# Kernel optimization log

Hardware: AMD Instinct MI355X
Metric: run time of the kernel (lower is better)

## Reference

```python
import jax, jax.numpy as jnp
import numpy as np

N_NODES = 100000
N_EDGES = 1600000


def setup_inputs() -> dict:
    key = jax.random.key(0)
    k1, k2, k3, k4 = jax.random.split(key, 4)
    x = jax.random.normal(k1, (N_NODES, 256), dtype=jnp.float32)
    edge_index = jax.random.randint(k2, (2, N_EDGES), 0, N_NODES, dtype=jnp.int64)
    W1 = jax.random.normal(k3, (256, 128), dtype=jnp.float32) * (1.0 / np.sqrt(256))
    W2 = jax.random.normal(k4, (128, 40), dtype=jnp.float32) * (1.0 / np.sqrt(128))
    return {"x": x, "edge_index": edge_index, "W1": W1, "W2": W2}


def _gcn_conv(x, W, src, dst):
    # GCNConv(normalize=False, add_self_loops=False, bias=False):
    # linear transform then sum-aggregate messages along edges src->dst.
    h = x @ W                                   # [N, d_out]
    msg = h[src]                                # [E, d_out] gather
    return jax.ops.segment_sum(msg, dst, num_segments=N_NODES)  # [N, d_out] scatter-add


def reference(x, edge_index, W1, W2):
    src, dst = edge_index[0], edge_index[1]
    h = jax.nn.relu(_gcn_conv(x, W1, src, dst))
    # dropout is identity in eval mode
    out = _gcn_conv(h, W2, src, dst)
    return out
```

## Files before the change

### kernel.cpp

```cpp
#include <hip/hip_runtime.h>

constexpr int NN = 100000;
constexpr int NE = 1600000;
constexpr int DI = 256, DH = 128, DO = 40;

constexpr int NB = (NN + 255) >> 8;
constexpr int NB_BLK = 512;
constexpr int CHUNK = NE / NB_BLK;
constexpr int M2 = NB * NB_BLK;
constexpr int NBS = (M2 + 1023) / 1024;
constexpr int STAGE_CAP = 6144;
constexpr int WPACK_BLOCKS = 152;
constexpr int GEMM1_BLOCKS = (NN + 63) / 64;

typedef __attribute__((ext_vector_type(8))) __bf16 bf16x8;
typedef __attribute__((ext_vector_type(4))) float f32x4;

__device__ inline float4 bf4_to_f4(ushort4 u) {
    return make_float4(__builtin_bit_cast(float, (unsigned)u.x << 16),
                       __builtin_bit_cast(float, (unsigned)u.y << 16),
                       __builtin_bit_cast(float, (unsigned)u.z << 16),
                       __builtin_bit_cast(float, (unsigned)u.w << 16));
}
__device__ inline unsigned short f2bf(float f) {
    return __builtin_bit_cast(unsigned short, (__bf16)f);
}
__device__ inline bf16x8 bf16x8_zero() {
    bf16x8 r;
    #pragma unroll
    for (int j = 0; j < 8; ++j) r[j] = (__bf16)0.f;
    return r;
}
__device__ inline bf16x8 load_cvt_a(const float* __restrict__ p, bool ok) {
    if (!ok) return bf16x8_zero();
    bf16x8 r;
    const float4 v0 = *(const float4*)p;
    const float4 v1 = *(const float4*)(p + 4);
    r[0] = (__bf16)v0.x; r[1] = (__bf16)v0.y; r[2] = (__bf16)v0.z; r[3] = (__bf16)v0.w;
    r[4] = (__bf16)v1.x; r[5] = (__bf16)v1.y; r[6] = (__bf16)v1.z; r[7] = (__bf16)v1.w;
    return r;
}
__device__ inline void acc4(float4& a, float4 v) {
    a.x += v.x; a.y += v.y; a.z += v.z; a.w += v.w;
}

__global__ __launch_bounds__(256) void wpack_hist_kernel(const float* __restrict__ W1,
                                                         const float* __restrict__ W2,
                                                         const int* __restrict__ dst,
                                                         __bf16* __restrict__ Wf,
                                                         __bf16* __restrict__ Wf2,
                                                         int* __restrict__ hist2d) {
    __shared__ int h[NB];
    if (blockIdx.x < 128) {
        const int i = blockIdx.x * 256 + threadIdx.x;
        const int j = i & 7;
        const int lane = (i >> 3) & 63;
        const int nt = (i >> 9) & 7;
        const int kt = i >> 12;
        const int k = kt * 32 + (lane >> 4) * 8 + j;
        const int n = nt * 16 + (lane & 15);
        Wf[i] = (__bf16)W1[(size_t)k * DH + n];
    } else if (blockIdx.x < WPACK_BLOCKS) {
        const int i = (blockIdx.x - 128) * 256 + threadIdx.x;
        if (i < 6144) {
            const int j = i & 7;
            const int lane = (i >> 3) & 63;
            const int g = i >> 9;
            const int nt = g % 3, ks = g / 3;
            const int k = ks * 32 + (lane >> 4) * 8 + j;
            const int n = nt * 16 + (lane & 15);
            Wf2[i] = (n < DO) ? (__bf16)W2[(size_t)k * DO + n] : (__bf16)0.f;
        }
    } else {
        const int hb = blockIdx.x - WPACK_BLOCKS;
        for (int i = threadIdx.x; i < NB; i += 256) h[i] = 0;
        __syncthreads();
        const int base = hb * CHUNK;
        for (int i = threadIdx.x; i < CHUNK; i += 256)
            atomicAdd(&h[dst[base + i] >> 8], 1);
        __syncthreads();
        for (int i = threadIdx.x; i < NB; i += 256)
            hist2d[i * NB_BLK + hb] = h[i];
    }
}

__global__ __launch_bounds__(256) void gemm1_scan_kernel(const float* __restrict__ x,
                                                         const __bf16* __restrict__ Wf,
                                                         __bf16* __restrict__ h1,
                                                         const int* __restrict__ hist2d,
                                                         int* __restrict__ offs2d) {
    __shared__ __bf16 wlds[32768];
    if (blockIdx.x >= NBS) {
        const int t = threadIdx.x;
        const int wave = t >> 6, lane = t & 63;
        const int q = lane >> 4, m = lane & 15;
        const int row0 = (blockIdx.x - NBS) * 64 + wave * 16;
        const int r = row0 + m;
        const bool ok = r < NN;
        const float* xp = x + (size_t)r * DI;

        bf16x8 a[8];
        #pragma unroll
        for (int kt = 0; kt < 8; ++kt)
            a[kt] = load_cvt_a(xp + kt * 32 + q * 8, ok);

        bf16x8* wl = (bf16x8*)wlds;
        const bf16x8* wfv = (const bf16x8*)Wf;
        #pragma unroll
        for (int i = 0; i < 16; ++i)
            wl[t + i * 256] = wfv[t + i * 256];

        f32x4 acc[8];
        #pragma unroll
        for (int nt = 0; nt < 8; ++nt)
            #pragma unroll
            for (int rr = 0; rr < 4; ++rr) acc[nt][rr] = 0.f;

        __syncthreads();

        #pragma unroll
        for (int kt = 0; kt < 8; ++kt) {
            #pragma unroll
            for (int nt = 0; nt < 8; ++nt) {
                const bf16x8 b = wl[(kt * 8 + nt) * 64 + lane];
                acc[nt] = __builtin_amdgcn_mfma_f32_16x16x32_bf16(a[kt], b, acc[nt], 0, 0, 0);
            }
        }
        #pragma unroll
        for (int reg = 0; reg < 4; ++reg) {
            const int rr = row0 + q * 4 + reg;
            if (rr < NN) {
                __bf16* hp = h1 + (size_t)rr * DH + m;
                #pragma unroll
                for (int nt = 0; nt < 8; ++nt) hp[nt * 16] = (__bf16)acc[nt][reg];
            }
        }
    } else {
        int* red = (int*)wlds;
        const int b = blockIdx.x;
        const int t = threadIdx.x;
        int s = 0;
        const int limit = b * 1024;
        for (int i = t * 4; i < limit; i += 1024) {
            const int4 v = *(const int4*)(hist2d + i);
            s += v.x + v.y + v.z + v.w;
        }
        red[t] = s;
        __syncthreads();
        #pragma unroll
        for (int d = 128; d > 0; d >>= 1) {
            if (t < d) red[t] += red[t + d];
            __syncthreads();
        }
        const int base = red[0];
        __syncthreads();
        const int idx = b * 1024 + t * 4;
        int4 v = make_int4(0, 0, 0, 0);
        if (idx < M2) v = *(const int4*)(hist2d + idx);
        const int sl = v.x + v.y + v.z + v.w;
        red[t] = sl;
        __syncthreads();
        for (int d = 1; d < 256; d <<= 1) {
            const int u = (t >= d) ? red[t - d] : 0;
            __syncthreads();
            red[t] += u;
            __syncthreads();
        }
        if (idx < M2) {
            const int e0 = base + red[t] - sl;
            *(int4*)(offs2d + idx) = make_int4(e0, e0 + v.x, e0 + v.x + v.y,
                                               e0 + v.x + v.y + v.z);
        }
    }
}

__global__ __launch_bounds__(256) void bucket_scatter_kernel(const int* __restrict__ src,
                                                             const int* __restrict__ dst,
                                                             const int* __restrict__ offs2d,
                                                             unsigned* __restrict__ epack) {
    __shared__ int cur[NB];
    for (int i = threadIdx.x; i < NB; i += 256)
        cur[i] = offs2d[i * NB_BLK + blockIdx.x];
    __syncthreads();
    const int base = blockIdx.x * CHUNK;
    for (int i = threadIdx.x; i < CHUNK; i += 256) {
        const int d = dst[base + i], s = src[base + i];
        const int p = atomicAdd(&cur[d >> 8], 1);
        epack[p] = (unsigned)s | ((unsigned)(d & 255) << 24);
    }
}

__global__ __launch_bounds__(256) void bucket_sort_kernel(const unsigned* __restrict__ epack,
                                                          const int* __restrict__ offs2d,
                                                          int* __restrict__ off,
                                                          int* __restrict__ esrc) {
    __shared__ int cnt[256];
    __shared__ int incl[256];
    __shared__ int cur[256];
    __shared__ int stage[STAGE_CAP];
    const int b = blockIdx.x;
    const int t = threadIdx.x;
    const int bstart = offs2d[b * NB_BLK];
    const int bend = (b + 1 < NB) ? offs2d[(b + 1) * NB_BLK] : NE;
    const int n = bend - bstart;
    cnt[t] = 0;
    __syncthreads();
    for (int i = t; i < n; i += 256)
        atomicAdd(&cnt[epack[bstart + i] >> 24], 1);
    __syncthreads();
    incl[t] = cnt[t];
    __syncthreads();
    for (int d = 1; d < 256; d <<= 1) {
        const int u = (t >= d) ? incl[t - d] : 0;
        __syncthreads();
        incl[t] += u;
        __syncthreads();
    }
    const int ex = incl[t] - cnt[t];
    const int node = (b << 8) + t;
    if (node <= NN) off[node] = bstart + ex;
    cur[t] = ex;
    __syncthreads();
    const bool staged = (n <= STAGE_CAP);
    for (int i = t; i < n; i += 256) {
        const unsigned pk = epack[bstart + i];
        const int p = atomicAdd(&cur[pk >> 24], 1);
        const int s = (int)(pk & 0xFFFFFFu);
        if (staged) stage[p] = s;
        else esrc[bstart + p] = s;
    }
    __syncthreads();
    if (staged)
        for (int i = t; i < n; i += 256) esrc[bstart + i] = stage[i];
}

__global__ __launch_bounds__(256) void agg1_kernel(const __bf16* __restrict__ h1,
                                                   const int* __restrict__ esrc,
                                                   const int* __restrict__ off,
                                                   __bf16* __restrict__ agg) {
    const int w = (blockIdx.x * 256 + threadIdx.x) >> 6;
    if (w >= NN) return;
    const int lane = threadIdx.x & 63;
    const int half = lane >> 5;
    const int c = (lane & 31) * 4;
    const int b = off[w], e = off[w + 1];
    float4 a0 = make_float4(0.f, 0.f, 0.f, 0.f);
    float4 a1 = a0, a2 = a0, a3 = a0;
    int j = b + half;
    for (; j + 6 < e; j += 8) {
        const int s0 = esrc[j], s1 = esrc[j + 2], s2 = esrc[j + 4], s3 = esrc[j + 6];
        acc4(a0, bf4_to_f4(*(const ushort4*)(h1 + (size_t)s0 * DH + c)));
        acc4(a1, bf4_to_f4(*(const ushort4*)(h1 + (size_t)s1 * DH + c)));
        acc4(a2, bf4_to_f4(*(const ushort4*)(h1 + (size_t)s2 * DH + c)));
        acc4(a3, bf4_to_f4(*(const ushort4*)(h1 + (size_t)s3 * DH + c)));
    }
    for (; j < e; j += 2) {
        const int s = esrc[j];
        acc4(a0, bf4_to_f4(*(const ushort4*)(h1 + (size_t)s * DH + c)));
    }
    float4 acc = make_float4(a0.x + a1.x + a2.x + a3.x,
                             a0.y + a1.y + a2.y + a3.y,
                             a0.z + a1.z + a2.z + a3.z,
                             a0.w + a1.w + a2.w + a3.w);
    acc.x += __shfl_xor(acc.x, 32);
    acc.y += __shfl_xor(acc.y, 32);
    acc.z += __shfl_xor(acc.z, 32);
    acc.w += __shfl_xor(acc.w, 32);
    if (half == 0) {
        ushort4 o;
        o.x = f2bf(fmaxf(acc.x, 0.f));
        o.y = f2bf(fmaxf(acc.y, 0.f));
        o.z = f2bf(fmaxf(acc.z, 0.f));
        o.w = f2bf(fmaxf(acc.w, 0.f));
        *(ushort4*)(agg + (size_t)w * DH + c) = o;
    }
}

__global__ __launch_bounds__(256) void gemm2_kernel(const __bf16* __restrict__ agg,
                                                    const __bf16* __restrict__ Wf2,
                                                    __bf16* __restrict__ h2) {
    const int t = threadIdx.x;
    const int wave = t >> 6, lane = t & 63;
    const int q = lane >> 4, m = lane & 15;
    const int row0 = blockIdx.x * 64 + wave * 16;
    const int r = row0 + m;
    const bool ok = r < NN;
    const __bf16* ap = agg + (size_t)r * DH;

    f32x4 acc[3];
    #pragma unroll
    for (int nt = 0; nt < 3; ++nt)
        #pragma unroll
        for (int rr = 0; rr < 4; ++rr) acc[nt][rr] = 0.f;

    const bf16x8* wf2 = (const bf16x8*)Wf2;
    #pragma unroll
    for (int ks = 0; ks < 4; ++ks) {
        const int k0 = ks * 32 + q * 8;
        const bf16x8 a = ok ? *(const bf16x8*)(ap + k0) : bf16x8_zero();
        #pragma unroll
        for (int nt = 0; nt < 3; ++nt) {
            const bf16x8 b = wf2[(ks * 3 + nt) * 64 + lane];
            acc[nt] = __builtin_amdgcn_mfma_f32_16x16x32_bf16(a, b, acc[nt], 0, 0, 0);
        }
    }
    #pragma unroll
    for (int reg = 0; reg < 4; ++reg) {
        const int rr = row0 + q * 4 + reg;
        if (rr < NN) {
            #pragma unroll
            for (int nt = 0; nt < 3; ++nt) {
                const int cc = nt * 16 + m;
                if (cc < DO) h2[(size_t)rr * DO + cc] = (__bf16)acc[nt][reg];
            }
        }
    }
}

__global__ __launch_bounds__(256) void agg2_kernel(const __bf16* __restrict__ h2,
                                                   const int* __restrict__ esrc,
                                                   const int* __restrict__ off,
                                                   float* __restrict__ out) {
    const int w = (blockIdx.x * 256 + threadIdx.x) >> 6;
    if (w >= NN) return;
    const int lane = threadIdx.x & 63;
    const int sub = lane / 10;
    const int c = (lane % 10) * 4;
    const int b = off[w], e = off[w + 1];
    const int deg = e - b;
    float4 a0 = make_float4(0.f, 0.f, 0.f, 0.f);
    float4 a1 = a0, a2 = a0, a3 = a0;

    for (int base = 0; base < deg; base += 64) {
        const int cnt = min(64, deg - base);
        const int cl = cnt - 1;
        const int idx = (base + lane < deg) ? esrc[b + base + lane] : 0;
        const bool act = sub < 6;
        int kk = 0;
        for (; kk + 24 <= cnt; kk += 24) {
            const int e0 = kk + sub;
            const int s0 = __shfl(idx, min(e0, cl));
            const int s1 = __shfl(idx, min(e0 + 6, cl));
            const int s2 = __shfl(idx, min(e0 + 12, cl));
            const int s3 = __shfl(idx, min(e0 + 18, cl));
            const float4 v0 = bf4_to_f4(*(const ushort4*)(h2 + (size_t)s0 * DO + c));
            const float4 v1 = bf4_to_f4(*(const ushort4*)(h2 + (size_t)s1 * DO + c));
            const float4 v2 = bf4_to_f4(*(const ushort4*)(h2 + (size_t)s2 * DO + c));
            const float4 v3 = bf4_to_f4(*(const ushort4*)(h2 + (size_t)s3 * DO + c));
            if (act) { acc4(a0, v0); acc4(a1, v1); acc4(a2, v2); acc4(a3, v3); }
        }
        for (; kk + 12 <= cnt; kk += 12) {
            const int e0 = kk + sub;
            const int s0 = __shfl(idx, min(e0, cl));
            const int s1 = __shfl(idx, min(e0 + 6, cl));
            const float4 v0 = bf4_to_f4(*(const ushort4*)(h2 + (size_t)s0 * DO + c));
            const float4 v1 = bf4_to_f4(*(const ushort4*)(h2 + (size_t)s1 * DO + c));
            if (act) { acc4(a0, v0); acc4(a1, v1); }
        }
        for (; kk < cnt; kk += 6) {
            const int e0 = kk + sub;
            const int s0 = __shfl(idx, min(e0, cl));
            const float4 v = bf4_to_f4(*(const ushort4*)(h2 + (size_t)s0 * DO + c));
            if (act && e0 < cnt) acc4(a0, v);
        }
    }
    float4 acc = make_float4(a0.x + a1.x + a2.x + a3.x, a0.y + a1.y + a2.y + a3.y,
                             a0.z + a1.z + a2.z + a3.z, a0.w + a1.w + a2.w + a3.w);
    acc.x += __shfl(acc.x, lane + 30);
    acc.y += __shfl(acc.y, lane + 30);
    acc.z += __shfl(acc.z, lane + 30);
    acc.w += __shfl(acc.w, lane + 30);
    const float ax = acc.x + __shfl(acc.x, lane + 10) + __shfl(acc.x, lane + 20);
    const float ay = acc.y + __shfl(acc.y, lane + 10) + __shfl(acc.y, lane + 20);
    const float az = acc.z + __shfl(acc.z, lane + 10) + __shfl(acc.z, lane + 20);
    const float aw = acc.w + __shfl(acc.w, lane + 10) + __shfl(acc.w, lane + 20);
    if (lane < 10) {
        *(float4*)(out + (size_t)w * DO + c) = make_float4(ax, ay, az, aw);
    }
}

extern "C" void kernel_launch(void* const* d_in, const int* in_sizes, int n_in,
                              void* d_out, int out_size, void* d_ws, size_t ws_size,
                              hipStream_t stream) {
    const float* x  = (const float*)d_in[0];
    const int*   ei = (const int*)d_in[1];
    const float* W1 = (const float*)d_in[2];
    const float* W2 = (const float*)d_in[3];
    const int* src = ei;
    const int* dst = ei + NE;

    __bf16* Wf  = (__bf16*)d_ws;
    __bf16* Wf2 = Wf + 32768;
    __bf16* h1  = Wf2 + 6144;
    __bf16* agg = h1 + (size_t)NN * DH;
    __bf16* h2  = h1;
    unsigned* epack = (unsigned*)(agg + (size_t)NN * DH);
    int* esrc   = (int*)(epack + NE);
    int* off    = esrc + NE;
    int* hist2d = off + NN + 1;
    int* offs2d = hist2d + M2;

    float* out = (float*)d_out;

    wpack_hist_kernel<<<WPACK_BLOCKS + NB_BLK, 256, 0, stream>>>(W1, W2, dst, Wf, Wf2, hist2d);
    gemm1_scan_kernel<<<GEMM1_BLOCKS + NBS, 256, 0, stream>>>(x, Wf, h1, hist2d, offs2d);
    bucket_scatter_kernel<<<NB_BLK, 256, 0, stream>>>(src, dst, offs2d, epack);
    bucket_sort_kernel<<<NB, 256, 0, stream>>>(epack, offs2d, off, esrc);
    agg1_kernel<<<(NN * 64 + 255) / 256, 256, 0, stream>>>(h1, esrc, off, agg);
    gemm2_kernel<<<(NN + 63) / 64, 256, 0, stream>>>(agg, Wf2, h2);
    agg2_kernel<<<(NN * 64 + 255) / 256, 256, 0, stream>>>(h2, esrc, off, out);
}
```

Before: 335.7 us.

## Spread GEMM1 blocks across scan, scatter and sort launches to overlap work

GEMM1 row blocks are split into three groups, and each group is folded into one of the scan, bucket-scatter and bucket-sort launches through a templated mid_kernel. The aim is to fill idle CUs during the small, latency-bound CSR-building phases with independent GEMM work, instead of running GEMM1 only alongside the scan. The cost is that every block now reserves 64KB of shared memory, which can lower occupancy for the scatter and sort blocks. The group sizes G0 and G1 are hand-tuned splits.

```diff
diff --git a/kernel.cpp b/kernel.cpp
--- a/kernel.cpp
+++ b/kernel.cpp
@@ -12,6 +12,10 @@
 constexpr int STAGE_CAP = 6144;
 constexpr int WPACK_BLOCKS = 152;
 constexpr int GEMM1_BLOCKS = (NN + 63) / 64;
+
+constexpr int G0 = 170;
+constexpr int G1 = 600;
+constexpr int G2 = GEMM1_BLOCKS - G0 - G1;
 
 typedef __attribute__((ext_vector_type(8))) __bf16 bf16x8;
 typedef __attribute__((ext_vector_type(4))) float f32x4;
@@ -84,105 +88,103 @@
     }
 }
 
-__global__ __launch_bounds__(256) void gemm1_scan_kernel(const float* __restrict__ x,
-                                                         const __bf16* __restrict__ Wf,
-                                                         __bf16* __restrict__ h1,
-                                                         const int* __restrict__ hist2d,
-                                                         int* __restrict__ offs2d) {
-    __shared__ __bf16 wlds[32768];
-    if (blockIdx.x >= NBS) {
-        const int t = threadIdx.x;
-        const int wave = t >> 6, lane = t & 63;
-        const int q = lane >> 4, m = lane & 15;
-        const int row0 = (blockIdx.x - NBS) * 64 + wave * 16;
-        const int r = row0 + m;
-        const bool ok = r < NN;
-        const float* xp = x + (size_t)r * DI;
-
-        bf16x8 a[8];
+
+__device__ inline void gemm1_body(f32x4* smem4, const float* __restrict__ x,
+                                  const __bf16* __restrict__ Wf,
+                                  __bf16* __restrict__ h1, int gb) {
+    const int t = threadIdx.x;
+    const int wave = t >> 6, lane = t & 63;
+    const int q = lane >> 4, m = lane & 15;
+    const int row0 = gb * 64 + wave * 16;
+    const int r = row0 + m;
+    const bool ok = r < NN;
+    const float* xp = x + (size_t)r * DI;
+
+    bf16x8 a[8];
+    #pragma unroll
+    for (int kt = 0; kt < 8; ++kt)
+        a[kt] = load_cvt_a(xp + kt * 32 + q * 8, ok);
+
+    bf16x8* wl = (bf16x8*)smem4;
+    const bf16x8* wfv = (const bf16x8*)Wf;
+    #pragma unroll
+    for (int i = 0; i < 16; ++i)
+        wl[t + i * 256] = wfv[t + i * 256];
+
+    f32x4 acc[8];
+    #pragma unroll
+    for (int nt = 0; nt < 8; ++nt)
         #pragma unroll
-        for (int kt = 0; kt < 8; ++kt)
-            a[kt] = load_cvt_a(xp + kt * 32 + q * 8, ok);
-
-        bf16x8* wl = (bf16x8*)wlds;
-        const bf16x8* wfv = (const bf16x8*)Wf;
+        for (int rr = 0; rr < 4; ++rr) acc[nt][rr] = 0.f;
+
+    __syncthreads();
+
+    #pragma unroll
+    for (int kt = 0; kt < 8; ++kt) {
         #pragma unroll
-        for (int i = 0; i < 16; ++i)
-            wl[t + i * 256] = wfv[t + i * 256];
-
-        f32x4 acc[8];
-        #pragma unroll
-        for (int nt = 0; nt < 8; ++nt)
+        for (int nt = 0; nt < 8; ++nt) {
+            const bf16x8 b = wl[(kt * 8 + nt) * 64 + lane];
+            acc[nt] = __builtin_amdgcn_mfma_f32_16x16x32_bf16(a[kt], b, acc[nt], 0, 0, 0);
+        }
+    }
+    #pragma unroll
+    for (int reg = 0; reg < 4; ++reg) {
+        const int rr = row0 + q * 4 + reg;
+        if (rr < NN) {
+            __bf16* hp = h1 + (size_t)rr * DH + m;
             #pragma unroll
-            for (int rr = 0; rr < 4; ++rr) acc[nt][rr] = 0.f;
-
-        __syncthreads();
-
-        #pragma unroll
-        for (int kt = 0; kt < 8; ++kt) {
-            #pragma unroll
-            for (int nt = 0; nt < 8; ++nt) {
-                const bf16x8 b = wl[(kt * 8 + nt) * 64 + lane];
-                acc[nt] = __builtin_amdgcn_mfma_f32_16x16x32_bf16(a[kt], b, acc[nt], 0, 0, 0);
-            }
-        }
-        #pragma unroll
-        for (int reg = 0; reg < 4; ++reg) {
-            const int rr = row0 + q * 4 + reg;
-            if (rr < NN) {
-                __bf16* hp = h1 + (size_t)rr * DH + m;
-                #pragma unroll
-                for (int nt = 0; nt < 8; ++nt) hp[nt * 16] = (__bf16)acc[nt][reg];
-            }
-        }
-    } else {
-        int* red = (int*)wlds;
-        const int b = blockIdx.x;
-        const int t = threadIdx.x;
-        int s = 0;
-        const int limit = b * 1024;
-        for (int i = t * 4; i < limit; i += 1024) {
-            const int4 v = *(const int4*)(hist2d + i);
-            s += v.x + v.y + v.z + v.w;
-        }
-        red[t] = s;
-        __syncthreads();
-        #pragma unroll
-        for (int d = 128; d > 0; d >>= 1) {
-            if (t < d) red[t] += red[t + d];
-            __syncthreads();
-        }
-        const int base = red[0];
-        __syncthreads();
-        const int idx = b * 1024 + t * 4;
-        int4 v = make_int4(0, 0, 0, 0);
-        if (idx < M2) v = *(const int4*)(hist2d + idx);
-        const int sl = v.x + v.y + v.z + v.w;
-        red[t] = sl;
-        __syncthreads();
-        for (int d = 1; d < 256; d <<= 1) {
-            const int u = (t >= d) ? red[t - d] : 0;
-            __syncthreads();
-            red[t] += u;
-            __syncthreads();
-        }
-        if (idx < M2) {
-            const int e0 = base + red[t] - sl;
-            *(int4*)(offs2d + idx) = make_int4(e0, e0 + v.x, e0 + v.x + v.y,
-                                               e0 + v.x + v.y + v.z);
-        }
-    }
-}
-
-__global__ __launch_bounds__(256) void bucket_scatter_kernel(const int* __restrict__ src,
-                                                             const int* __restrict__ dst,
-                                                             const int* __restrict__ offs2d,
-                                                             unsigned* __restrict__ epack) {
-    __shared__ int cur[NB];
+            for (int nt = 0; nt < 8; ++nt) hp[nt * 16] = (__bf16)acc[nt][reg];
+        }
+    }
+}
+
+__device__ inline void scan_body(f32x4* smem4, const int* __restrict__ hist2d,
+                                 int* __restrict__ offs2d, int b) {
+    int* red = (int*)smem4;
+    const int t = threadIdx.x;
+    int s = 0;
+    const int limit = b * 1024;
+    for (int i = t * 4; i < limit; i += 1024) {
+        const int4 v = *(const int4*)(hist2d + i);
+        s += v.x + v.y + v.z + v.w;
+    }
+    red[t] = s;
+    __syncthreads();
+    #pragma unroll
+    for (int d = 128; d > 0; d >>= 1) {
+        if (t < d) red[t] += red[t + d];
+        __syncthreads();
+    }
+    const int base = red[0];
+    __syncthreads();
+    const int idx = b * 1024 + t * 4;
+    int4 v = make_int4(0, 0, 0, 0);
+    if (idx < M2) v = *(const int4*)(hist2d + idx);
+    const int sl = v.x + v.y + v.z + v.w;
+    red[t] = sl;
+    __syncthreads();
+    for (int d = 1; d < 256; d <<= 1) {
+        const int u = (t >= d) ? red[t - d] : 0;
+        __syncthreads();
+        red[t] += u;
+        __syncthreads();
+    }
+    if (idx < M2) {
+        const int e0 = base + red[t] - sl;
+        *(int4*)(offs2d + idx) = make_int4(e0, e0 + v.x, e0 + v.x + v.y,
+                                           e0 + v.x + v.y + v.z);
+    }
+}
+
+__device__ inline void scatter_body(f32x4* smem4, const int* __restrict__ src,
+                                    const int* __restrict__ dst,
+                                    const int* __restrict__ offs2d,
+                                    unsigned* __restrict__ epack, int hb) {
+    int* cur = (int*)smem4;
     for (int i = threadIdx.x; i < NB; i += 256)
-        cur[i] = offs2d[i * NB_BLK + blockIdx.x];
-    __syncthreads();
-    const int base = blockIdx.x * CHUNK;
+        cur[i] = offs2d[i * NB_BLK + hb];
+    __syncthreads();
+    const int base = hb * CHUNK;
     for (int i = threadIdx.x; i < CHUNK; i += 256) {
         const int d = dst[base + i], s = src[base + i];
         const int p = atomicAdd(&cur[d >> 8], 1);
@@ -190,15 +192,13 @@
     }
 }
 
-__global__ __launch_bounds__(256) void bucket_sort_kernel(const unsigned* __restrict__ epack,
-                                                          const int* __restrict__ offs2d,
-                                                          int* __restrict__ off,
-                                                          int* __restrict__ esrc) {
-    __shared__ int cnt[256];
-    __shared__ int incl[256];
-    __shared__ int cur[256];
-    __shared__ int stage[STAGE_CAP];
-    const int b = blockIdx.x;
+__device__ inline void sort_body(f32x4* smem4, const unsigned* __restrict__ epack,
+                                 const int* __restrict__ offs2d,
+                                 int* __restrict__ off, int* __restrict__ esrc, int b) {
+    int* cnt  = (int*)smem4;
+    int* incl = cnt + 256;
+    int* cur  = incl + 256;
+    int* stage = cur + 256;
     const int t = threadIdx.x;
     const int bstart = offs2d[b * NB_BLK];
     const int bend = (b + 1 < NB) ? offs2d[(b + 1) * NB_BLK] : NE;
@@ -232,6 +232,28 @@
     __syncthreads();
     if (staged)
         for (int i = t; i < n; i += 256) esrc[bstart + i] = stage[i];
+}
+
+template<int PHASE, int CHAIN, int GBASE>
+__global__ __launch_bounds__(256) void mid_kernel(const float* __restrict__ x,
+                                                  const __bf16* __restrict__ Wf,
+                                                  __bf16* __restrict__ h1,
+                                                  const int* __restrict__ hist2d,
+                                                  int* __restrict__ offs2d,
+                                                  const int* __restrict__ src,
+                                                  const int* __restrict__ dst,
+                                                  unsigned* __restrict__ epack,
+                                                  int* __restrict__ off,
+                                                  int* __restrict__ esrc) {
+    __shared__ f32x4 smem4[4096];
+    const int b = blockIdx.x;
+    if (b < CHAIN) {
+        if constexpr (PHASE == 0) scan_body(smem4, hist2d, offs2d, b);
+        else if constexpr (PHASE == 1) scatter_body(smem4, src, dst, offs2d, epack, b);
+        else sort_body(smem4, epack, offs2d, off, esrc, b);
+    } else {
+        gemm1_body(smem4, x, Wf, h1, GBASE + (b - CHAIN));
+    }
 }
 
 __global__ __launch_bounds__(256) void agg1_kernel(const __bf16* __restrict__ h1,
@@ -403,9 +425,12 @@
     float* out = (float*)d_out;
 
     wpack_hist_kernel<<<WPACK_BLOCKS + NB_BLK, 256, 0, stream>>>(W1, W2, dst, Wf, Wf2, hist2d);
-    gemm1_scan_kernel<<<GEMM1_BLOCKS + NBS, 256, 0, stream>>>(x, Wf, h1, hist2d, offs2d);
-    bucket_scatter_kernel<<<NB_BLK, 256, 0, stream>>>(src, dst, offs2d, epack);
-    bucket_sort_kernel<<<NB, 256, 0, stream>>>(epack, offs2d, off, esrc);
+    mid_kernel<0, NBS, 0><<<NBS + G0, 256, 0, stream>>>(
+        x, Wf, h1, hist2d, offs2d, src, dst, epack, off, esrc);
+    mid_kernel<1, NB_BLK, G0><<<NB_BLK + G1, 256, 0, stream>>>(
+        x, Wf, h1, hist2d, offs2d, src, dst, epack, off, esrc);
+    mid_kernel<2, NB, G0 + G1><<<NB + G2, 256, 0, stream>>>(
+        x, Wf, h1, hist2d, offs2d, src, dst, epack, off, esrc);
     agg1_kernel<<<(NN * 64 + 255) / 256, 256, 0, stream>>>(h1, esrc, off, agg);
     gemm2_kernel<<<(NN + 63) / 64, 256, 0, stream>>>(agg, Wf2, h2);
     agg2_kernel<<<(NN * 64 + 255) / 256, 256, 0, stream>>>(h2, esrc, off, out);
```

Measured after the change: 358.0 us. 1.07x slower.

## Replace two-pass bucket sort CSR build with global atomic count and scatter

Applied to the files above, without the earlier changes.

Replaces the bucketed two-level sort (per-block bucket histograms, bucket scatter, per-bucket local sort) with a direct per-node global atomic histogram, a flat scan over node counts, and a scatter using global atomic cursors. This removes one kernel launch and the intermediate packed edge buffer. The cost is many contended global atomics and random scattered writes. Edge order within each node also becomes nondeterministic, which changes float summation order.

```diff
diff --git a/kernel.cpp b/kernel.cpp
--- a/kernel.cpp
+++ b/kernel.cpp
@@ -4,14 +4,12 @@
 constexpr int NE = 1600000;
 constexpr int DI = 256, DH = 128, DO = 40;
 
-constexpr int NB = (NN + 255) >> 8;
-constexpr int NB_BLK = 512;
-constexpr int CHUNK = NE / NB_BLK;
-constexpr int M2 = NB * NB_BLK;
-constexpr int NBS = (M2 + 1023) / 1024;
-constexpr int STAGE_CAP = 6144;
 constexpr int WPACK_BLOCKS = 152;
+constexpr int ZERO_BLOCKS = (NN + 255) / 256;
+constexpr int NBS2 = (NN + 1023) / 1024;
 constexpr int GEMM1_BLOCKS = (NN + 63) / 64;
+constexpr int HIST_BLOCKS = 1024;
+constexpr int SCAT_BLOCKS = 1024;
 
 typedef __attribute__((ext_vector_type(8))) __bf16 bf16x8;
 typedef __attribute__((ext_vector_type(4))) float f32x4;
@@ -44,13 +42,12 @@
     a.x += v.x; a.y += v.y; a.z += v.z; a.w += v.w;
 }
 
-__global__ __launch_bounds__(256) void wpack_hist_kernel(const float* __restrict__ W1,
+__global__ __launch_bounds__(256) void wpack_zero_kernel(const float* __restrict__ W1,
                                                          const float* __restrict__ W2,
-                                                         const int* __restrict__ dst,
                                                          __bf16* __restrict__ Wf,
                                                          __bf16* __restrict__ Wf2,
-                                                         int* __restrict__ hist2d) {
-    __shared__ int h[NB];
+                                                         int* __restrict__ cnt,
+                                                         int* __restrict__ off) {
     if (blockIdx.x < 128) {
         const int i = blockIdx.x * 256 + threadIdx.x;
         const int j = i & 7;
@@ -72,29 +69,36 @@
             Wf2[i] = (n < DO) ? (__bf16)W2[(size_t)k * DO + n] : (__bf16)0.f;
         }
     } else {
-        const int hb = blockIdx.x - WPACK_BLOCKS;
-        for (int i = threadIdx.x; i < NB; i += 256) h[i] = 0;
-        __syncthreads();
-        const int base = hb * CHUNK;
-        for (int i = threadIdx.x; i < CHUNK; i += 256)
-            atomicAdd(&h[dst[base + i] >> 8], 1);
-        __syncthreads();
-        for (int i = threadIdx.x; i < NB; i += 256)
-            hist2d[i * NB_BLK + hb] = h[i];
+        const int i = (blockIdx.x - WPACK_BLOCKS) * 256 + threadIdx.x;
+        if (i < NN) cnt[i] = 0;
+        else if (i == NN) off[NN] = NE;
+    }
+}
+
+__global__ __launch_bounds__(256) void hist_kernel(const int* __restrict__ dst,
+                                                   int* __restrict__ cnt) {
+    const int stride = HIST_BLOCKS * 256;
+    for (int i = blockIdx.x * 256 + threadIdx.x; i < NE / 4; i += stride) {
+        const int4 d = ((const int4*)dst)[i];
+        atomicAdd(&cnt[d.x], 1);
+        atomicAdd(&cnt[d.y], 1);
+        atomicAdd(&cnt[d.z], 1);
+        atomicAdd(&cnt[d.w], 1);
     }
 }
 
 __global__ __launch_bounds__(256) void gemm1_scan_kernel(const float* __restrict__ x,
                                                          const __bf16* __restrict__ Wf,
                                                          __bf16* __restrict__ h1,
-                                                         const int* __restrict__ hist2d,
-                                                         int* __restrict__ offs2d) {
+                                                         const int* __restrict__ cnt,
+                                                         int* __restrict__ off,
+                                                         int* __restrict__ cur) {
     __shared__ __bf16 wlds[32768];
-    if (blockIdx.x >= NBS) {
+    if (blockIdx.x >= NBS2) {
         const int t = threadIdx.x;
         const int wave = t >> 6, lane = t & 63;
         const int q = lane >> 4, m = lane & 15;
-        const int row0 = (blockIdx.x - NBS) * 64 + wave * 16;
+        const int row0 = (blockIdx.x - NBS2) * 64 + wave * 16;
         const int r = row0 + m;
         const bool ok = r < NN;
         const float* xp = x + (size_t)r * DI;
@@ -142,7 +146,7 @@
         int s = 0;
         const int limit = b * 1024;
         for (int i = t * 4; i < limit; i += 1024) {
-            const int4 v = *(const int4*)(hist2d + i);
+            const int4 v = *(const int4*)(cnt + i);
             s += v.x + v.y + v.z + v.w;
         }
         red[t] = s;
@@ -156,7 +160,7 @@
         __syncthreads();
         const int idx = b * 1024 + t * 4;
         int4 v = make_int4(0, 0, 0, 0);
-        if (idx < M2) v = *(const int4*)(hist2d + idx);
+        if (idx < NN) v = *(const int4*)(cnt + idx);
         const int sl = v.x + v.y + v.z + v.w;
         red[t] = sl;
         __syncthreads();
@@ -166,72 +170,30 @@
             red[t] += u;
             __syncthreads();
         }
-        if (idx < M2) {
+        if (idx < NN) {
             const int e0 = base + red[t] - sl;
-            *(int4*)(offs2d + idx) = make_int4(e0, e0 + v.x, e0 + v.x + v.y,
-                                               e0 + v.x + v.y + v.z);
-        }
-    }
-}
-
-__global__ __launch_bounds__(256) void bucket_scatter_kernel(const int* __restrict__ src,
-                                                             const int* __restrict__ dst,
-                                                             const int* __restrict__ offs2d,
-                                                             unsigned* __restrict__ epack) {
-    __shared__ int cur[NB];
-    for (int i = threadIdx.x; i < NB; i += 256)
-        cur[i] = offs2d[i * NB_BLK + blockIdx.x];
-    __syncthreads();
-    const int base = blockIdx.x * CHUNK;
-    for (int i = threadIdx.x; i < CHUNK; i += 256) {
-        const int d = dst[base + i], s = src[base + i];
-        const int p = atomicAdd(&cur[d >> 8], 1);
-        epack[p] = (unsigned)s | ((unsigned)(d & 255) << 24);
-    }
-}
-
-__global__ __launch_bounds__(256) void bucket_sort_kernel(const unsigned* __restrict__ epack,
-                                                          const int* __restrict__ offs2d,
-                                                          int* __restrict__ off,
-                                                          int* __restrict__ esrc) {
-    __shared__ int cnt[256];
-    __shared__ int incl[256];
-    __shared__ int cur[256];
-    __shared__ int stage[STAGE_CAP];
-    const int b = blockIdx.x;
-    const int t = threadIdx.x;
-    const int bstart = offs2d[b * NB_BLK];
-    const int bend = (b + 1 < NB) ? offs2d[(b + 1) * NB_BLK] : NE;
-    const int n = bend - bstart;
-    cnt[t] = 0;
-    __syncthreads();
-    for (int i = t; i < n; i += 256)
-        atomicAdd(&cnt[epack[bstart + i] >> 24], 1);
-    __syncthreads();
-    incl[t] = cnt[t];
-    __syncthreads();
-    for (int d = 1; d < 256; d <<= 1) {
-        const int u = (t >= d) ? incl[t - d] : 0;
-        __syncthreads();
-        incl[t] += u;
-        __syncthreads();
-    }
-    const int ex = incl[t] - cnt[t];
-    const int node = (b << 8) + t;
-    if (node <= NN) off[node] = bstart + ex;
-    cur[t] = ex;
-    __syncthreads();
-    const bool staged = (n <= STAGE_CAP);
-    for (int i = t; i < n; i += 256) {
-        const unsigned pk = epack[bstart + i];
-        const int p = atomicAdd(&cur[pk >> 24], 1);
-        const int s = (int)(pk & 0xFFFFFFu);
-        if (staged) stage[p] = s;
-        else esrc[bstart + p] = s;
-    }
-    __syncthreads();
-    if (staged)
-        for (int i = t; i < n; i += 256) esrc[bstart + i] = stage[i];
+            const int4 o = make_int4(e0, e0 + v.x, e0 + v.x + v.y,
+                                     e0 + v.x + v.y + v.z);
+            *(int4*)(off + idx) = o;
+            *(int4*)(cur + idx) = o;
+        }
+    }
+}
+
+__global__ __launch_bounds__(256) void scatter_kernel(const int* __restrict__ src,
+                                                      const int* __restrict__ dst,
+                                                      int* __restrict__ cur,
+                                                      int* __restrict__ esrc) {
+    const int stride = SCAT_BLOCKS * 256;
+    for (int i = blockIdx.x * 256 + threadIdx.x; i < NE / 4; i += stride) {
+        const int4 d = ((const int4*)dst)[i];
+        const int4 s = ((const int4*)src)[i];
+        int p;
+        p = atomicAdd(&cur[d.x], 1); esrc[p] = s.x;
+        p = atomicAdd(&cur[d.y], 1); esrc[p] = s.y;
+        p = atomicAdd(&cur[d.z], 1); esrc[p] = s.z;
+        p = atomicAdd(&cur[d.w], 1); esrc[p] = s.w;
+    }
 }
 
 __global__ __launch_bounds__(256) void agg1_kernel(const __bf16* __restrict__ h1,
@@ -394,18 +356,19 @@
     __bf16* h1  = Wf2 + 6144;
     __bf16* agg = h1 + (size_t)NN * DH;
     __bf16* h2  = h1;
-    unsigned* epack = (unsigned*)(agg + (size_t)NN * DH);
-    int* esrc   = (int*)(epack + NE);
+    int* esrc   = (int*)(agg + (size_t)NN * DH);
     int* off    = esrc + NE;
-    int* hist2d = off + NN + 1;
-    int* offs2d = hist2d + M2;
+    int* cnt    = off + NN + 1;
+    int* cur    = cnt + NN;
 
     float* out = (float*)d_out;
 
-    wpack_hist_kernel<<<WPACK_BLOCKS + NB_BLK, 256, 0, stream>>>(W1, W2, dst, Wf, Wf2, hist2d);
-    gemm1_scan_kernel<<<GEMM1_BLOCKS + NBS, 256, 0, stream>>>(x, Wf, h1, hist2d, offs2d);
-    bucket_scatter_kernel<<<NB_BLK, 256, 0, stream>>>(src, dst, offs2d, epack);
-    bucket_sort_kernel<<<NB, 256, 0, stream>>>(epack, offs2d, off, esrc);
+    wpack_zero_kernel<<<WPACK_BLOCKS + ZERO_BLOCKS, 256, 0, stream>>>(
+        W1, W2, Wf, Wf2, cnt, off);
+    hist_kernel<<<HIST_BLOCKS, 256, 0, stream>>>(dst, cnt);
+    gemm1_scan_kernel<<<GEMM1_BLOCKS + NBS2, 256, 0, stream>>>(
+        x, Wf, h1, cnt, off, cur);
+    scatter_kernel<<<SCAT_BLOCKS, 256, 0, stream>>>(src, dst, cur, esrc);
     agg1_kernel<<<(NN * 64 + 255) / 256, 256, 0, stream>>>(h1, esrc, off, agg);
     gemm2_kernel<<<(NN + 63) / 64, 256, 0, stream>>>(agg, Wf2, h2);
     agg2_kernel<<<(NN * 64 + 255) / 256, 256, 0, stream>>>(h2, esrc, off, out);
```

Measured after the change: 447.7 us. 1.33x slower.

## Fuse layer-1 aggregation with layer-2 GEMM via shared-memory row tile

Applied to the files above, without the earlier changes.

Merges the first-layer gather/sum/ReLU kernel and the second-layer MFMA GEMM into one kernel. Each block aggregates 16 nodes (4 per wave) into an LDS tile, then three waves run the 16x16x32 bf16 MFMA against W2. This removes the round trip of the 100000x128 bf16 aggregate through global memory and one kernel launch. In exchange each wave now handles 4 nodes in sequence rather than 1, and one wave sits idle during the GEMM phase, which may reduce memory-level parallelism in the gather.

```diff
diff --git a/kernel.cpp b/kernel.cpp
--- a/kernel.cpp
+++ b/kernel.cpp
@@ -234,84 +234,74 @@
         for (int i = t; i < n; i += 256) esrc[bstart + i] = stage[i];
 }
 
-__global__ __launch_bounds__(256) void agg1_kernel(const __bf16* __restrict__ h1,
-                                                   const int* __restrict__ esrc,
-                                                   const int* __restrict__ off,
-                                                   __bf16* __restrict__ agg) {
-    const int w = (blockIdx.x * 256 + threadIdx.x) >> 6;
-    if (w >= NN) return;
-    const int lane = threadIdx.x & 63;
+__global__ __launch_bounds__(256) void agg1g2_kernel(const __bf16* __restrict__ h1,
+                                                     const int* __restrict__ esrc,
+                                                     const int* __restrict__ off,
+                                                     const __bf16* __restrict__ Wf2,
+                                                     __bf16* __restrict__ h2) {
+    __shared__ __bf16 rows[16][136];
+    const int t = threadIdx.x;
+    const int wave = t >> 6, lane = t & 63;
     const int half = lane >> 5;
     const int c = (lane & 31) * 4;
-    const int b = off[w], e = off[w + 1];
-    float4 a0 = make_float4(0.f, 0.f, 0.f, 0.f);
-    float4 a1 = a0, a2 = a0, a3 = a0;
-    int j = b + half;
-    for (; j + 6 < e; j += 8) {
-        const int s0 = esrc[j], s1 = esrc[j + 2], s2 = esrc[j + 4], s3 = esrc[j + 6];
-        acc4(a0, bf4_to_f4(*(const ushort4*)(h1 + (size_t)s0 * DH + c)));
-        acc4(a1, bf4_to_f4(*(const ushort4*)(h1 + (size_t)s1 * DH + c)));
-        acc4(a2, bf4_to_f4(*(const ushort4*)(h1 + (size_t)s2 * DH + c)));
-        acc4(a3, bf4_to_f4(*(const ushort4*)(h1 + (size_t)s3 * DH + c)));
-    }
-    for (; j < e; j += 2) {
-        const int s = esrc[j];
-        acc4(a0, bf4_to_f4(*(const ushort4*)(h1 + (size_t)s * DH + c)));
-    }
-    float4 acc = make_float4(a0.x + a1.x + a2.x + a3.x,
-                             a0.y + a1.y + a2.y + a3.y,
-                             a0.z + a1.z + a2.z + a3.z,
-                             a0.w + a1.w + a2.w + a3.w);
-    acc.x += __shfl_xor(acc.x, 32);
-    acc.y += __shfl_xor(acc.y, 32);
-    acc.z += __shfl_xor(acc.z, 32);
-    acc.w += __shfl_xor(acc.w, 32);
-    if (half == 0) {
-        ushort4 o;
-        o.x = f2bf(fmaxf(acc.x, 0.f));
-        o.y = f2bf(fmaxf(acc.y, 0.f));
-        o.z = f2bf(fmaxf(acc.z, 0.f));
-        o.w = f2bf(fmaxf(acc.w, 0.f));
-        *(ushort4*)(agg + (size_t)w * DH + c) = o;
-    }
-}
-
-__global__ __launch_bounds__(256) void gemm2_kernel(const __bf16* __restrict__ agg,
-                                                    const __bf16* __restrict__ Wf2,
-                                                    __bf16* __restrict__ h2) {
-    const int t = threadIdx.x;
-    const int wave = t >> 6, lane = t & 63;
-    const int q = lane >> 4, m = lane & 15;
-    const int row0 = blockIdx.x * 64 + wave * 16;
-    const int r = row0 + m;
-    const bool ok = r < NN;
-    const __bf16* ap = agg + (size_t)r * DH;
-
-    f32x4 acc[3];
-    #pragma unroll
-    for (int nt = 0; nt < 3; ++nt)
-        #pragma unroll
-        for (int rr = 0; rr < 4; ++rr) acc[nt][rr] = 0.f;
-
-    const bf16x8* wf2 = (const bf16x8*)Wf2;
-    #pragma unroll
-    for (int ks = 0; ks < 4; ++ks) {
-        const int k0 = ks * 32 + q * 8;
-        const bf16x8 a = ok ? *(const bf16x8*)(ap + k0) : bf16x8_zero();
-        #pragma unroll
-        for (int nt = 0; nt < 3; ++nt) {
+    const int node0 = blockIdx.x * 16;
+
+    for (int k = 0; k < 4; ++k) {
+        const int r = wave * 4 + k;
+        const int w = node0 + r;
+        const int b = off[w], e = off[w + 1];
+        float4 a0 = make_float4(0.f, 0.f, 0.f, 0.f);
+        float4 a1 = a0, a2 = a0, a3 = a0;
+        int j = b + half;
+        for (; j + 6 < e; j += 8) {
+            const int s0 = esrc[j], s1 = esrc[j + 2], s2 = esrc[j + 4], s3 = esrc[j + 6];
+            acc4(a0, bf4_to_f4(*(const ushort4*)(h1 + (size_t)s0 * DH + c)));
+            acc4(a1, bf4_to_f4(*(const ushort4*)(h1 + (size_t)s1 * DH + c)));
+            acc4(a2, bf4_to_f4(*(const ushort4*)(h1 + (size_t)s2 * DH + c)));
+            acc4(a3, bf4_to_f4(*(const ushort4*)(h1 + (size_t)s3 * DH + c)));
+        }
+        for (; j < e; j += 2) {
+            const int s = esrc[j];
+            acc4(a0, bf4_to_f4(*(const ushort4*)(h1 + (size_t)s * DH + c)));
+        }
+        float4 acc = make_float4(a0.x + a1.x + a2.x + a3.x,
+                                 a0.y + a1.y + a2.y + a3.y,
+                                 a0.z + a1.z + a2.z + a3.z,
+                                 a0.w + a1.w + a2.w + a3.w);
+        acc.x += __shfl_xor(acc.x, 32);
+        acc.y += __shfl_xor(acc.y, 32);
+        acc.z += __shfl_xor(acc.z, 32);
+        acc.w += __shfl_xor(acc.w, 32);
+        if (half == 0) {
+            ushort4 o;
+            o.x = f2bf(fmaxf(acc.x, 0.f));
+            o.y = f2bf(fmaxf(acc.y, 0.f));
+            o.z = f2bf(fmaxf(acc.z, 0.f));
+            o.w = f2bf(fmaxf(acc.w, 0.f));
+            *(ushort4*)(&rows[r][c]) = o;
+        }
+    }
+    __syncthreads();
+
+    if (wave < 3) {
+        const int nt = wave;
+        const int q = lane >> 4, m = lane & 15;
+        f32x4 acc;
+        #pragma unroll
+        for (int rr = 0; rr < 4; ++rr) acc[rr] = 0.f;
+        const bf16x8* wf2 = (const bf16x8*)Wf2;
+        #pragma unroll
+        for (int ks = 0; ks < 4; ++ks) {
+            const bf16x8 a = *(const bf16x8*)(&rows[m][ks * 32 + q * 8]);
             const bf16x8 b = wf2[(ks * 3 + nt) * 64 + lane];
-            acc[nt] = __builtin_amdgcn_mfma_f32_16x16x32_bf16(a, b, acc[nt], 0, 0, 0);
-        }
-    }
-    #pragma unroll
-    for (int reg = 0; reg < 4; ++reg) {
-        const int rr = row0 + q * 4 + reg;
-        if (rr < NN) {
+            acc = __builtin_amdgcn_mfma_f32_16x16x32_bf16(a, b, acc, 0, 0, 0);
+        }
+        const int cc = nt * 16 + m;
+        if (cc < DO) {
             #pragma unroll
-            for (int nt = 0; nt < 3; ++nt) {
-                const int cc = nt * 16 + m;
-                if (cc < DO) h2[(size_t)rr * DO + cc] = (__bf16)acc[nt][reg];
+            for (int reg = 0; reg < 4; ++reg) {
+                const int rr = node0 + q * 4 + reg;
+                h2[(size_t)rr * DO + cc] = (__bf16)acc[reg];
             }
         }
     }
@@ -392,9 +382,8 @@
     __bf16* Wf  = (__bf16*)d_ws;
     __bf16* Wf2 = Wf + 32768;
     __bf16* h1  = Wf2 + 6144;
-    __bf16* agg = h1 + (size_t)NN * DH;
-    __bf16* h2  = h1;
-    unsigned* epack = (unsigned*)(agg + (size_t)NN * DH);
+    __bf16* h2  = h1 + (size_t)NN * DH;
+    unsigned* epack = (unsigned*)(h2 + (size_t)NN * DO);
     int* esrc   = (int*)(epack + NE);
     int* off    = esrc + NE;
     int* hist2d = off + NN + 1;
@@ -406,7 +395,6 @@
     gemm1_scan_kernel<<<GEMM1_BLOCKS + NBS, 256, 0, stream>>>(x, Wf, h1, hist2d, offs2d);
     bucket_scatter_kernel<<<NB_BLK, 256, 0, stream>>>(src, dst, offs2d, epack);
     bucket_sort_kernel<<<NB, 256, 0, stream>>>(epack, offs2d, off, esrc);
-    agg1_kernel<<<(NN * 64 + 255) / 256, 256, 0, stream>>>(h1, esrc, off, agg);
-    gemm2_kernel<<<(NN + 63) / 64, 256, 0, stream>>>(agg, Wf2, h2);
+    agg1g2_kernel<<<NN / 16, 256, 0, stream>>>(h1, esrc, off, Wf2, h2);
     agg2_kernel<<<(NN * 64 + 255) / 256, 256, 0, stream>>>(h2, esrc, off, out);
 }
```

Measured after the change: 329.6 us (median of 2 runs). No clear change (-1.8%).
